# Optimization experiments

Measured on AMD Instinct MI355X. Metric: run time of the kernel, lower is better.

Reference implementation:

```python
import jax, jax.numpy as jnp
import numpy as np

# Dims: module math forces per-head depth D == num_points == N (see analysis).
B, H, N = 4, 8, 1024
D = N                      # q_depth = k_depth = v_depth = num_points
C_IN = 64                  # q_in = k_in = v_in
C_OUT = H * D              # q_out = k_out = v_out = 8192
SCALE = float(np.sqrt(D))


def _split_heads(t):
    # t: [B, C_OUT, N] -> view(B, H, D, N) -> permute -> [B, H, N, D]
    return t.reshape(B, H, D, N).transpose(0, 1, 3, 2)


def setup_inputs() -> dict:
    key = jax.random.key(0)
    ks = jax.random.split(key, 9)
    s = 0.02
    return {
        "coordinate": jax.random.normal(ks[0], (B, 3, N), jnp.float32),
        "x": jax.random.normal(ks[1], (B, C_IN, N, 1), jnp.float32),
        "neighbors": jax.random.normal(ks[2], (B, C_IN, N, 1), jnp.float32),
        # 1x1 Conv2d weights (out, in), no bias
        "Wq": jax.random.normal(ks[3], (C_OUT, C_IN), jnp.float32) * s,
        "Wk": jax.random.normal(ks[4], (C_OUT, C_IN), jnp.float32) * s,
        "Wv": jax.random.normal(ks[5], (C_OUT, C_IN), jnp.float32) * s,
        # nn.Linear(3, q_out) / nn.Linear(3, v_out)
        "Wlq": jax.random.normal(ks[6], (C_OUT, 3), jnp.float32) * s,
        "blq": jnp.zeros((C_OUT,), jnp.float32),
        "Wlv": jax.random.normal(ks[7], (C_OUT, 3), jnp.float32) * s,
        "blv": jnp.zeros((C_OUT,), jnp.float32),
    }


def reference(coordinate, x, neighbors, Wq, Wk, Wv, Wlq, blq, Wlv, blv):
    # Att_Score_method='dot_product', pos_method='method_ii' (hardcoded branch)
    xs = x[..., 0]           # [B, C_IN, N]  (squeeze trailing Conv2d width dim)
    ns = neighbors[..., 0]   # [B, C_IN, N]

    q = _split_heads(jnp.einsum('oc,bcn->bon', Wq, xs))  # [B,H,N,D]
    k = _split_heads(jnp.einsum('oc,bcn->bon', Wk, ns))  # [B,H,N,D]
    v = _split_heads(jnp.einsum('oc,bcn->bon', Wv, ns))  # [B,H,N,D]

    coords = coordinate.transpose(0, 2, 1)               # [B, N, 3]
    # positional encodings, split into heads: [B,H,N,D]
    pos_q = _split_heads((coords @ Wlq.T + blq).transpose(0, 2, 1))
    pos_v = _split_heads((coords @ Wlv.T + blv).transpose(0, 2, 1))

    # q_context = q @ pos_q^T ; energy = q @ k^T + q_context  -> [B,H,N,N]
    q_context = jnp.einsum('bhnd,bhmd->bhnm', q, pos_q)
    energy = jnp.einsum('bhnd,bhmd->bhnm', q, k) + q_context

    attn = jax.nn.softmax(energy / SCALE, axis=-1)       # [B,H,N,N]
    v_context = v + pos_v                                 # [B,H,N,D], D==N
    out = attn * v_context                                # elementwise combine

    # permute(0,2,1,3) -> [B,N,H,D] -> reshape [B,N,H*D] -> permute -> [B,H*D,N]
    out = out.transpose(0, 2, 1, 3).reshape(B, N, H * D).transpose(0, 2, 1)
    return out
```

## Files before the change

### kernel.cpp

```cpp
#include <hip/hip_runtime.h>

#define NN 1024
#define KP 96
#define LSTR 104

typedef __attribute__((ext_vector_type(8))) short short8;
typedef __attribute__((ext_vector_type(4))) short short4v;
typedef __attribute__((ext_vector_type(4))) float f32x4;

__device__ __forceinline__ short f2bf(float f){
  unsigned u = __builtin_bit_cast(unsigned, f);
  u += 0x7FFFu + ((u >> 16) & 1u);
  return (short)(u >> 16);
}

__global__ __launch_bounds__(256) void prep_all(
    const float* __restrict__ Wq, const float* __restrict__ Wk,
    const float* __restrict__ Wlq, const float* __restrict__ blq,
    const float* __restrict__ ns, const float* __restrict__ coord,
    const float* __restrict__ Wv, const float* __restrict__ Wlv,
    const float* __restrict__ blv,
    short* __restrict__ PTbf, short* __restrict__ Bm, short* __restrict__ Vm){
  __shared__ union SU {
    float red[4][64][9];
    struct { float nsT[64][65]; float cst[3][64]; } bb;
  } S;
  const int t = threadIdx.x;
  const int r = blockIdx.x;

  if (r < 96){
    const int h = r / 12, kidx = r % 12, kk0 = kidx * 8;
    const int c = t & 63, p = t >> 6;
    if (kidx > 8){
      if (p == 0){
        #pragma unroll
        for (int j = 0; j < 8; ++j) PTbf[(h*96 + kk0 + j)*64 + c] = 0;
      }
      return;
    }
    float acc[8];
    #pragma unroll
    for (int j = 0; j < 8; ++j) acc[j] = 0.f;
    if (kidx < 8){
      #pragma unroll 4
      for (int i = 0; i < 256; ++i){
        const int o = h*1024 + p*256 + i;
        const float wq = Wq[o*64 + c];
        const float* wk = Wk + o*64 + kk0;
        f32x4 b0 = *(const f32x4*)(wk);
        f32x4 b1 = *(const f32x4*)(wk + 4);
        #pragma unroll
        for (int j = 0; j < 4; ++j){ acc[j] += wq*b0[j]; acc[4+j] += wq*b1[j]; }
      }
    } else {
      #pragma unroll 4
      for (int i = 0; i < 256; ++i){
        const int o = h*1024 + p*256 + i;
        const float wq = Wq[o*64 + c];
        acc[0] += wq * Wlq[o*3 + 0];
        acc[1] += wq * Wlq[o*3 + 1];
        acc[2] += wq * Wlq[o*3 + 2];
        acc[3] += wq * blq[o];
      }
    }
    #pragma unroll
    for (int j = 0; j < 8; ++j) S.red[p][c][j] = acc[j];
    __syncthreads();
    if (p == 0){
      #pragma unroll
      for (int j = 0; j < 8; ++j){
        float s = S.red[0][c][j] + S.red[1][c][j] + S.red[2][c][j] + S.red[3][c][j];
        PTbf[(h*96 + kk0 + j)*64 + c] = f2bf(s);
      }
    }
  } else if (r < 160){
    const int rb = r - 96;
    const int b = rb >> 4, m0 = (rb & 15) * 64;
    #pragma unroll
    for (int it = 0; it < 16; ++it){
      int idx = it * 256 + t;
      int c = idx >> 6, mm = idx & 63;
      S.bb.nsT[mm][c] = ns[(b*64 + c)*NN + m0 + mm];
    }
    if (t < 192){
      int j = t >> 6, mm = t & 63;
      S.bb.cst[j][mm] = coord[(b*3 + j)*NN + m0 + mm];
    }
    __syncthreads();
    #pragma unroll
    for (int it = 0; it < 24; ++it){
      int idx = it * 256 + t;
      int mm = idx / KP, kk = idx - mm*KP;
      float v = (kk < 64) ? S.bb.nsT[mm][kk]
              : (kk < 67) ? S.bb.cst[kk - 64][mm]
              : (kk == 67) ? 1.f : 0.f;
      Bm[(b*NN + m0 + mm)*KP + kk] = f2bf(v);
    }
  } else {
    const int o0 = (r - 160) * 64;
    #pragma unroll
    for (int it = 0; it < 24; ++it){
      int idx = it * 256 + t;
      int rr = idx / KP, kk = idx - rr*KP;
      int o = o0 + rr;
      float v = (kk < 64) ? Wv[o*64 + kk]
              : (kk < 67) ? Wlv[o*3 + (kk - 64)]
              : (kk == 67) ? blv[o] : 0.f;
      Vm[o*KP + kk] = f2bf(v);
    }
  }
}

__global__ __launch_bounds__(256) void attn_main(
    const float* __restrict__ xs, const short* __restrict__ PTbf,
    const short* __restrict__ Bmat, const short* __restrict__ Vm,
    float* __restrict__ out){
  __shared__ short xsL[64 * 64];
  __shared__ short AL[64 * LSTR];
  __shared__ float redS[64 * 4];
  const int t = threadIdx.x, w = t >> 6, lane = t & 63;
  const int q = lane >> 4, ln = lane & 15;
  const int blk = blockIdx.x, nb = blk & 15, bh = blk >> 4;
  const int b = bh >> 3, h = bh & 7;
  const int n0 = nb * 64;

  const float* xsb = xs + b * 64 * NN;
  #pragma unroll
  for (int it = 0; it < 4; ++it){
    int idx = it * 256 + t;
    int c = idx >> 4, nn4 = (idx & 15) << 2;
    f32x4 v = *(const f32x4*)(xsb + c * NN + n0 + nn4);
    short4v pk;
    #pragma unroll
    for (int j = 0; j < 4; ++j) pk[j] = f2bf(v[j]);
    *(short4v*)(&xsL[c * 64 + nn4]) = pk;
  }
  __syncthreads();

  short8 xf0, xf1;
  #pragma unroll
  for (int j = 0; j < 8; ++j){
    xf0[j] = xsL[(q * 8 + j) * 64 + w * 16 + ln];
    xf1[j] = xsL[(32 + q * 8 + j) * 64 + w * 16 + ln];
  }
  const short* PTh = PTbf + h * KP * 64;
  #pragma unroll
  for (int kt = 0; kt < 6; ++kt){
    const short* pr = PTh + (kt * 16 + ln) * 64;
    short8 p0 = *(const short8*)(pr + q * 8);
    short8 p1 = *(const short8*)(pr + 32 + q * 8);
    f32x4 a = {0.f, 0.f, 0.f, 0.f};
    a = __builtin_amdgcn_mfma_f32_16x16x32_bf16(xf0, p0, a, 0, 0, 0);
    a = __builtin_amdgcn_mfma_f32_16x16x32_bf16(xf1, p1, a, 0, 0, 0);
    #pragma unroll
    for (int r = 0; r < 4; ++r)
      AL[(w * 16 + q * 4 + r) * LSTR + kt * 16 + ln] = f2bf(a[r]);
  }
  __syncthreads();

  short8 af[4][3], bn[4][3];
  const short* Bb = Bmat + b * NN * KP;
  #pragma unroll
  for (int rf = 0; rf < 4; ++rf){
    #pragma unroll
    for (int s = 0; s < 3; ++s){
      af[rf][s] = *(const short8*)(&AL[(rf * 16 + ln) * LSTR + s * 32 + q * 8]);
      bn[rf][s] = *(const short8*)(Bb + (n0 + rf * 16 + ln) * KP + s * 32 + q * 8);
    }
  }
  const float KEXP = 0.045084220f;

  float sum[4][4];
  #pragma unroll
  for (int rf = 0; rf < 4; ++rf)
    #pragma unroll
    for (int r = 0; r < 4; ++r) sum[rf][r] = 0.f;

  short8 bf0, bf1, bf2;
  {
    const short* bp = Bb + (w * 256 + ln) * KP + q * 8;
    bf0 = *(const short8*)(bp);
    bf1 = *(const short8*)(bp + 32);
    bf2 = *(const short8*)(bp + 64);
  }
  for (int ms = 0; ms < 16; ++ms){
    short8 nb0, nb1, nb2;
    {
      int msn = (ms + 1) & 15;
      const short* bp = Bb + (w * 256 + msn * 16 + ln) * KP + q * 8;
      nb0 = *(const short8*)(bp);
      nb1 = *(const short8*)(bp + 32);
      nb2 = *(const short8*)(bp + 64);
    }
    #pragma unroll
    for (int rf = 0; rf < 4; ++rf){
      f32x4 e = {0.f, 0.f, 0.f, 0.f};
      e = __builtin_amdgcn_mfma_f32_16x16x32_bf16(af[rf][0], bf0, e, 0, 0, 0);
      e = __builtin_amdgcn_mfma_f32_16x16x32_bf16(af[rf][1], bf1, e, 0, 0, 0);
      e = __builtin_amdgcn_mfma_f32_16x16x32_bf16(af[rf][2], bf2, e, 0, 0, 0);
      #pragma unroll
      for (int r = 0; r < 4; ++r)
        sum[rf][r] += __builtin_amdgcn_exp2f(e[r] * KEXP);
    }
    bf0 = nb0; bf1 = nb1; bf2 = nb2;
  }
  #pragma unroll
  for (int rf = 0; rf < 4; ++rf){
    #pragma unroll
    for (int r = 0; r < 4; ++r){
      float s = sum[rf][r];
      s += __shfl_xor(s, 1); s += __shfl_xor(s, 2);
      s += __shfl_xor(s, 4); s += __shfl_xor(s, 8);
      sum[rf][r] = s;
    }
  }
  if (ln == 0){
    #pragma unroll
    for (int rf = 0; rf < 4; ++rf)
      #pragma unroll
      for (int r = 0; r < 4; ++r)
        redS[(rf * 16 + q * 4 + r) * 4 + w] = sum[rf][r];
  }
  __syncthreads();
  float rinv[4][4];
  #pragma unroll
  for (int rf = 0; rf < 4; ++rf){
    #pragma unroll
    for (int r = 0; r < 4; ++r){
      f32x4 v4 = *(const f32x4*)(&redS[(rf * 16 + q * 4 + r) * 4]);
      rinv[rf][r] = 1.0f / (v4[0] + v4[1] + v4[2] + v4[3]);
    }
  }

  float* outp = out + (size_t)bh * (1024 * 1024);
  const short* Vh = Vm + h * 1024 * KP;
  short8 vf0, vf1, vf2;
  {
    const short* bp = Bb + (w * 256 + ln) * KP + q * 8;
    const short* vp = Vh + (w * 256 + ln) * KP + q * 8;
    bf0 = *(const short8*)(bp); bf1 = *(const short8*)(bp + 32); bf2 = *(const short8*)(bp + 64);
    vf0 = *(const short8*)(vp); vf1 = *(const short8*)(vp + 32); vf2 = *(const short8*)(vp + 64);
  }
  for (int ds = 0; ds < 16; ++ds){
    int d0 = w * 256 + ds * 16;
    short8 nb0, nb1, nb2, nv0, nv1, nv2;
    {
      int dsn = (ds + 1) & 15;
      const short* bp = Bb + (w * 256 + dsn * 16 + ln) * KP + q * 8;
      const short* vp = Vh + (w * 256 + dsn * 16 + ln) * KP + q * 8;
      nb0 = *(const short8*)(bp); nb1 = *(const short8*)(bp + 32); nb2 = *(const short8*)(bp + 64);
      nv0 = *(const short8*)(vp); nv1 = *(const short8*)(vp + 32); nv2 = *(const short8*)(vp + 64);
    }
    #pragma unroll
    for (int rf = 0; rf < 4; ++rf){
      f32x4 e  = {0.f, 0.f, 0.f, 0.f};
      f32x4 vv = {0.f, 0.f, 0.f, 0.f};
      e  = __builtin_amdgcn_mfma_f32_16x16x32_bf16(af[rf][0], bf0, e, 0, 0, 0);
      e  = __builtin_amdgcn_mfma_f32_16x16x32_bf16(af[rf][1], bf1, e, 0, 0, 0);
      e  = __builtin_amdgcn_mfma_f32_16x16x32_bf16(af[rf][2], bf2, e, 0, 0, 0);
      vv = __builtin_amdgcn_mfma_f32_16x16x32_bf16(bn[rf][0], vf0, vv, 0, 0, 0);
      vv = __builtin_amdgcn_mfma_f32_16x16x32_bf16(bn[rf][1], vf1, vv, 0, 0, 0);
      vv = __builtin_amdgcn_mfma_f32_16x16x32_bf16(bn[rf][2], vf2, vv, 0, 0, 0);
      f32x4 o;
      #pragma unroll
      for (int r = 0; r < 4; ++r)
        o[r] = __builtin_amdgcn_exp2f(e[r] * KEXP) * rinv[rf][r] * vv[r];
      *(f32x4*)(outp + (d0 + ln) * NN + n0 + rf * 16 + q * 4) = o;
    }
    bf0 = nb0; bf1 = nb1; bf2 = nb2;
    vf0 = nv0; vf1 = nv1; vf2 = nv2;
  }
}

extern "C" void kernel_launch(void* const* d_in, const int* in_sizes, int n_in,
                              void* d_out, int out_size, void* d_ws, size_t ws_size,
                              hipStream_t stream){
  const float* coord = (const float*)d_in[0];
  const float* x     = (const float*)d_in[1];
  const float* nbr   = (const float*)d_in[2];
  const float* Wq    = (const float*)d_in[3];
  const float* Wk    = (const float*)d_in[4];
  const float* Wv    = (const float*)d_in[5];
  const float* Wlq   = (const float*)d_in[6];
  const float* blq   = (const float*)d_in[7];
  const float* Wlv   = (const float*)d_in[8];
  const float* blv   = (const float*)d_in[9];
  float* out = (float*)d_out;

  char* ws = (char*)d_ws;
  short* PTbf = (short*)ws;
  short* Bm   = (short*)(ws + 98304);
  short* Vm   = (short*)(ws + 98304 + 786432);

  prep_all<<<288, 256, 0, stream>>>(Wq, Wk, Wlq, blq, nbr, coord, Wv, Wlv, blv,
                                    PTbf, Bm, Vm);
  attn_main<<<512, 256, 0, stream>>>(x, PTbf, Bm, Vm, out);
}
```

Measured before the change: 219.7 us.

## Halve row tile to 32, double blocks, swizzle block order, drop manual prefetch

```diff
diff --git a/kernel.cpp b/kernel.cpp
--- a/kernel.cpp
+++ b/kernel.cpp
@@ -111,57 +111,63 @@
   }
 }
 
-__global__ __launch_bounds__(256) void attn_main(
+__global__ __launch_bounds__(256, 4) void attn_main(
     const float* __restrict__ xs, const short* __restrict__ PTbf,
     const short* __restrict__ Bmat, const short* __restrict__ Vm,
     float* __restrict__ out){
-  __shared__ short xsL[64 * 64];
-  __shared__ short AL[64 * LSTR];
-  __shared__ float redS[64 * 4];
+  __shared__ short xsL[64 * 32];
+  __shared__ short AL[32 * LSTR];
+  __shared__ float redS[32 * 4];
   const int t = threadIdx.x, w = t >> 6, lane = t & 63;
   const int q = lane >> 4, ln = lane & 15;
-  const int blk = blockIdx.x, nb = blk & 15, bh = blk >> 4;
+  const int blk0 = blockIdx.x;
+  const int blk = (blk0 & 7) * 128 + (blk0 >> 3);
+  const int nb = blk & 31, bh = blk >> 5;
   const int b = bh >> 3, h = bh & 7;
-  const int n0 = nb * 64;
+  const int n0 = nb * 32;
 
   const float* xsb = xs + b * 64 * NN;
   #pragma unroll
-  for (int it = 0; it < 4; ++it){
+  for (int it = 0; it < 2; ++it){
     int idx = it * 256 + t;
-    int c = idx >> 4, nn4 = (idx & 15) << 2;
+    int c = idx >> 3, nn4 = (idx & 7) << 2;
     f32x4 v = *(const f32x4*)(xsb + c * NN + n0 + nn4);
     short4v pk;
     #pragma unroll
     for (int j = 0; j < 4; ++j) pk[j] = f2bf(v[j]);
-    *(short4v*)(&xsL[c * 64 + nn4]) = pk;
+    *(short4v*)(&xsL[c * 32 + nn4]) = pk;
   }
   __syncthreads();
 
-  short8 xf0, xf1;
-  #pragma unroll
-  for (int j = 0; j < 8; ++j){
-    xf0[j] = xsL[(q * 8 + j) * 64 + w * 16 + ln];
-    xf1[j] = xsL[(32 + q * 8 + j) * 64 + w * 16 + ln];
-  }
-  const short* PTh = PTbf + h * KP * 64;
-  #pragma unroll
-  for (int kt = 0; kt < 6; ++kt){
-    const short* pr = PTh + (kt * 16 + ln) * 64;
-    short8 p0 = *(const short8*)(pr + q * 8);
-    short8 p1 = *(const short8*)(pr + 32 + q * 8);
-    f32x4 a = {0.f, 0.f, 0.f, 0.f};
-    a = __builtin_amdgcn_mfma_f32_16x16x32_bf16(xf0, p0, a, 0, 0, 0);
-    a = __builtin_amdgcn_mfma_f32_16x16x32_bf16(xf1, p1, a, 0, 0, 0);
-    #pragma unroll
-    for (int r = 0; r < 4; ++r)
-      AL[(w * 16 + q * 4 + r) * LSTR + kt * 16 + ln] = f2bf(a[r]);
+  {
+    const int rw = (w & 1) * 16, kh = w >> 1;
+    short8 xf0, xf1;
+    #pragma unroll
+    for (int j = 0; j < 8; ++j){
+      xf0[j] = xsL[(q * 8 + j) * 32 + rw + ln];
+      xf1[j] = xsL[(32 + q * 8 + j) * 32 + rw + ln];
+    }
+    const short* PTh = PTbf + h * KP * 64;
+    #pragma unroll
+    for (int j = 0; j < 3; ++j){
+      int kt = kh * 3 + j;
+      const short* pr = PTh + (kt * 16 + ln) * 64;
+      short8 p0 = *(const short8*)(pr + q * 8);
+      short8 p1 = *(const short8*)(pr + 32 + q * 8);
+      f32x4 a = {0.f, 0.f, 0.f, 0.f};
+      a = __builtin_amdgcn_mfma_f32_16x16x32_bf16(xf0, p0, a, 0, 0, 0);
+      a = __builtin_amdgcn_mfma_f32_16x16x32_bf16(xf1, p1, a, 0, 0, 0);
+      #pragma unroll
+      for (int r = 0; r < 4; ++r)
+        AL[(rw + q * 4 + r) * LSTR + kt * 16 + ln] = f2bf(a[r]);
+    }
   }
   __syncthreads();
 
-  short8 af[4][3], bn[4][3];
+  short8 af[2][3], bn[2][3];
   const short* Bb = Bmat + b * NN * KP;
   #pragma unroll
-  for (int rf = 0; rf < 4; ++rf){
+  for (int rf = 0; rf < 2; ++rf){
     #pragma unroll
     for (int s = 0; s < 3; ++s){
       af[rf][s] = *(const short8*)(&AL[(rf * 16 + ln) * LSTR + s * 32 + q * 8]);
@@ -170,61 +176,45 @@
   }
   const float KEXP = 0.045084220f;
 
-  float sum[4][4];
-  #pragma unroll
-  for (int rf = 0; rf < 4; ++rf)
+  float sum[2][4];
+  #pragma unroll
+  for (int rf = 0; rf < 2; ++rf)
     #pragma unroll
     for (int r = 0; r < 4; ++r) sum[rf][r] = 0.f;
 
-  short8 bf0, bf1, bf2;
   {
     const short* bp = Bb + (w * 256 + ln) * KP + q * 8;
-    bf0 = *(const short8*)(bp);
-    bf1 = *(const short8*)(bp + 32);
-    bf2 = *(const short8*)(bp + 64);
-  }
-  for (int ms = 0; ms < 16; ++ms){
-    short8 nb0, nb1, nb2;
-    {
-      int msn = (ms + 1) & 15;
-      const short* bp = Bb + (w * 256 + msn * 16 + ln) * KP + q * 8;
-      nb0 = *(const short8*)(bp);
-      nb1 = *(const short8*)(bp + 32);
-      nb2 = *(const short8*)(bp + 64);
-    }
-    #pragma unroll
-    for (int rf = 0; rf < 4; ++rf){
-      f32x4 e = {0.f, 0.f, 0.f, 0.f};
-      e = __builtin_amdgcn_mfma_f32_16x16x32_bf16(af[rf][0], bf0, e, 0, 0, 0);
-      e = __builtin_amdgcn_mfma_f32_16x16x32_bf16(af[rf][1], bf1, e, 0, 0, 0);
-      e = __builtin_amdgcn_mfma_f32_16x16x32_bf16(af[rf][2], bf2, e, 0, 0, 0);
-      #pragma unroll
-      for (int r = 0; r < 4; ++r)
-        sum[rf][r] += __builtin_amdgcn_exp2f(e[r] * KEXP);
-    }
-    bf0 = nb0; bf1 = nb1; bf2 = nb2;
-  }
-  #pragma unroll
-  for (int rf = 0; rf < 4; ++rf){
+    for (int ms = 0; ms < 16; ++ms){
+      short8 bf0 = *(const short8*)(bp);
+      short8 bf1 = *(const short8*)(bp + 32);
+      short8 bf2 = *(const short8*)(bp + 64);
+      bp += 16 * KP;
+      #pragma unroll
+      for (int rf = 0; rf < 2; ++rf){
+        f32x4 e = {0.f, 0.f, 0.f, 0.f};
+        e = __builtin_amdgcn_mfma_f32_16x16x32_bf16(af[rf][0], bf0, e, 0, 0, 0);
+        e = __builtin_amdgcn_mfma_f32_16x16x32_bf16(af[rf][1], bf1, e, 0, 0, 0);
+        e = __builtin_amdgcn_mfma_f32_16x16x32_bf16(af[rf][2], bf2, e, 0, 0, 0);
+        #pragma unroll
+        for (int r = 0; r < 4; ++r)
+          sum[rf][r] += __builtin_amdgcn_exp2f(e[r] * KEXP);
+      }
+    }
+  }
+  #pragma unroll
+  for (int rf = 0; rf < 2; ++rf){
     #pragma unroll
     for (int r = 0; r < 4; ++r){
       float s = sum[rf][r];
       s += __shfl_xor(s, 1); s += __shfl_xor(s, 2);
       s += __shfl_xor(s, 4); s += __shfl_xor(s, 8);
-      sum[rf][r] = s;
-    }
-  }
-  if (ln == 0){
-    #pragma unroll
-    for (int rf = 0; rf < 4; ++rf)
-      #pragma unroll
-      for (int r = 0; r < 4; ++r)
-        redS[(rf * 16 + q * 4 + r) * 4 + w] = sum[rf][r];
+      if (ln == 0) redS[(rf * 16 + q * 4 + r) * 4 + w] = s;
+    }
   }
   __syncthreads();
-  float rinv[4][4];
-  #pragma unroll
-  for (int rf = 0; rf < 4; ++rf){
+  float rinv[2][4];
+  #pragma unroll
+  for (int rf = 0; rf < 2; ++rf){
     #pragma unroll
     for (int r = 0; r < 4; ++r){
       f32x4 v4 = *(const f32x4*)(&redS[(rf * 16 + q * 4 + r) * 4]);
@@ -232,43 +222,37 @@
     }
   }
 
-  float* outp = out + (size_t)bh * (1024 * 1024);
-  const short* Vh = Vm + h * 1024 * KP;
-  short8 vf0, vf1, vf2;
   {
+    const short* Vh = Vm + h * 1024 * KP;
     const short* bp = Bb + (w * 256 + ln) * KP + q * 8;
     const short* vp = Vh + (w * 256 + ln) * KP + q * 8;
-    bf0 = *(const short8*)(bp); bf1 = *(const short8*)(bp + 32); bf2 = *(const short8*)(bp + 64);
-    vf0 = *(const short8*)(vp); vf1 = *(const short8*)(vp + 32); vf2 = *(const short8*)(vp + 64);
-  }
-  for (int ds = 0; ds < 16; ++ds){
-    int d0 = w * 256 + ds * 16;
-    short8 nb0, nb1, nb2, nv0, nv1, nv2;
-    {
-      int dsn = (ds + 1) & 15;
-      const short* bp = Bb + (w * 256 + dsn * 16 + ln) * KP + q * 8;
-      const short* vp = Vh + (w * 256 + dsn * 16 + ln) * KP + q * 8;
-      nb0 = *(const short8*)(bp); nb1 = *(const short8*)(bp + 32); nb2 = *(const short8*)(bp + 64);
-      nv0 = *(const short8*)(vp); nv1 = *(const short8*)(vp + 32); nv2 = *(const short8*)(vp + 64);
-    }
-    #pragma unroll
-    for (int rf = 0; rf < 4; ++rf){
-      f32x4 e  = {0.f, 0.f, 0.f, 0.f};
-      f32x4 vv = {0.f, 0.f, 0.f, 0.f};
-      e  = __builtin_amdgcn_mfma_f32_16x16x32_bf16(af[rf][0], bf0, e, 0, 0, 0);
-      e  = __builtin_amdgcn_mfma_f32_16x16x32_bf16(af[rf][1], bf1, e, 0, 0, 0);
-      e  = __builtin_amdgcn_mfma_f32_16x16x32_bf16(af[rf][2], bf2, e, 0, 0, 0);
-      vv = __builtin_amdgcn_mfma_f32_16x16x32_bf16(bn[rf][0], vf0, vv, 0, 0, 0);
-      vv = __builtin_amdgcn_mfma_f32_16x16x32_bf16(bn[rf][1], vf1, vv, 0, 0, 0);
-      vv = __builtin_amdgcn_mfma_f32_16x16x32_bf16(bn[rf][2], vf2, vv, 0, 0, 0);
-      f32x4 o;
-      #pragma unroll
-      for (int r = 0; r < 4; ++r)
-        o[r] = __builtin_amdgcn_exp2f(e[r] * KEXP) * rinv[rf][r] * vv[r];
-      *(f32x4*)(outp + (d0 + ln) * NN + n0 + rf * 16 + q * 4) = o;
-    }
-    bf0 = nb0; bf1 = nb1; bf2 = nb2;
-    vf0 = nv0; vf1 = nv1; vf2 = nv2;
+    float* op = out + (size_t)bh * (1024 * 1024) + (w * 256 + ln) * NN + n0;
+    for (int ds = 0; ds < 16; ++ds){
+      short8 bf0 = *(const short8*)(bp);
+      short8 bf1 = *(const short8*)(bp + 32);
+      short8 bf2 = *(const short8*)(bp + 64);
+      short8 vf0 = *(const short8*)(vp);
+      short8 vf1 = *(const short8*)(vp + 32);
+      short8 vf2 = *(const short8*)(vp + 64);
+      bp += 16 * KP; vp += 16 * KP;
+      #pragma unroll
+      for (int rf = 0; rf < 2; ++rf){
+        f32x4 e  = {0.f, 0.f, 0.f, 0.f};
+        f32x4 vv = {0.f, 0.f, 0.f, 0.f};
+        e  = __builtin_amdgcn_mfma_f32_16x16x32_bf16(af[rf][0], bf0, e, 0, 0, 0);
+        e  = __builtin_amdgcn_mfma_f32_16x16x32_bf16(af[rf][1], bf1, e, 0, 0, 0);
+        e  = __builtin_amdgcn_mfma_f32_16x16x32_bf16(af[rf][2], bf2, e, 0, 0, 0);
+        vv = __builtin_amdgcn_mfma_f32_16x16x32_bf16(bn[rf][0], vf0, vv, 0, 0, 0);
+        vv = __builtin_amdgcn_mfma_f32_16x16x32_bf16(bn[rf][1], vf1, vv, 0, 0, 0);
+        vv = __builtin_amdgcn_mfma_f32_16x16x32_bf16(bn[rf][2], vf2, vv, 0, 0, 0);
+        f32x4 o;
+        #pragma unroll
+        for (int r = 0; r < 4; ++r)
+          o[r] = __builtin_amdgcn_exp2f(e[r] * KEXP) * rinv[rf][r] * vv[r];
+        *(f32x4*)(op + rf * 16 + q * 4) = o;
+      }
+      op += 16 * NN;
+    }
   }
 }
 
@@ -294,5 +278,5 @@
 
   prep_all<<<288, 256, 0, stream>>>(Wq, Wk, Wlq, blq, nbr, coord, Wv, Wlv, blv,
                                     PTbf, Bm, Vm);
-  attn_main<<<512, 256, 0, stream>>>(x, PTbf, Bm, Vm, out);
-}
+  attn_main<<<1024, 256, 0, stream>>>(x, PTbf, Bm, Vm, out);
+}
```

Result: slower. 305.8 us (+39.2%).
